# Optimization experiments

Hardware: AMD Instinct MI355X
Metric: run time of the kernel (lower is better)

The kernel has to match this reference:

```python
import jax, jax.numpy as jnp
import numpy as np

B, N, D = 4, 1024, 512      # batch, seq (nodes), input_dim
DK, DV, NH = 512, 512, 8    # dim_k, dim_v, num_heads
EPS = 1e-5


def setup_inputs() -> dict:
    key = jax.random.key(0)
    ks = jax.random.split(key, 9)
    s = 1.0 / np.sqrt(D).astype(np.float32)
    return {
        "user_exo": jax.random.normal(ks[0], (B, N, D), jnp.float32),
        "exo": jax.random.normal(ks[1], (B, N, D), jnp.float32),
        "adj": jax.random.uniform(ks[2], (N, N), jnp.float32),
        "Wq": jax.random.normal(ks[3], (DK, D), jnp.float32) * s,
        "bq": jnp.zeros((DK,), jnp.float32),
        "Wk": jax.random.normal(ks[4], (DK, D), jnp.float32) * s,
        "bk": jnp.zeros((DK,), jnp.float32),
        "Wv": jax.random.normal(ks[5], (DV, D), jnp.float32) * s,
        "bv": jnp.zeros((DV,), jnp.float32),
        "gamma": jnp.ones((D,), jnp.float32),
        "beta": jnp.zeros((D,), jnp.float32),
    }


def reference(user_exo, exo, adj, Wq, bq, Wk, bk, Wv, bv, gamma, beta):
    # LayerNorm over last dim (eps=1e-5, affine)
    mu = jnp.mean(user_exo, axis=-1, keepdims=True)
    var = jnp.mean(jnp.square(user_exo - mu), axis=-1, keepdims=True)
    c = (user_exo - mu) * jax.lax.rsqrt(var + EPS) * gamma + beta

    dk, dv = DK // NH, DV // NH
    # projections -> [B, NH, N, dk/dv]
    q = (jnp.einsum('bnd,kd->bnk', c, Wq) + bq).reshape(B, N, NH, dk).transpose(0, 2, 1, 3)
    k = (jnp.einsum('bnd,kd->bnk', c, Wk) + bk).reshape(B, N, NH, dk).transpose(0, 2, 1, 3)
    v = (jnp.einsum('bnd,kd->bnk', exo, Wv) + bv).reshape(B, N, NH, dv).transpose(0, 2, 1, 3)

    # NOTE: original scales by 1/sqrt(dim_k) (full dim_k, not per-head)
    scale = 1.0 / np.sqrt(DK).astype(np.float32)
    scores = jnp.einsum('bhnd,bhmd->bhnm', q, k) * scale
    dist = jax.nn.softmax(scores, axis=-1)
    # post-softmax multiplicative adjacency mask (mask_local=False path)
    dist = adj * dist  # adj [N,N] broadcasts over [B,NH,N,N]

    att = jnp.einsum('bhnm,bhmd->bhnd', dist, v)
    att = att.transpose(0, 2, 1, 3).reshape(B, N, DV)
    return att, dist
```

## Files before the change

kernel.cpp:

```cpp
#include <hip/hip_runtime.h>
#include <hip/hip_bf16.h>

typedef __hip_bfloat16 bf16;
typedef short v8s __attribute__((ext_vector_type(8)));
typedef float v4f __attribute__((ext_vector_type(4)));

#define BB   4
#define NN   1024
#define DD   512
#define NHH  8
#define DH   64

__device__ __forceinline__ void split2(float v, bf16& hi, bf16& lo) {
    hi = __float2bfloat16(v);
    lo = __float2bfloat16(v - __bfloat162float(hi));
}

__device__ __forceinline__ short f2bf_bits(float f) {
    bf16 h = __float2bfloat16(f);
    short s;
    __builtin_memcpy(&s, &h, 2);
    return s;
}

__global__ __launch_bounds__(256) void ln_split_kernel(
    const float* __restrict__ x, const float* __restrict__ gamma,
    const float* __restrict__ beta,
    bf16* __restrict__ c_hi, bf16* __restrict__ c_lo)
{
    int row = blockIdx.x;
    int t = threadIdx.x;
    const float* xr = x + (size_t)row * DD;
    float v0 = xr[2 * t];
    float v1 = xr[2 * t + 1];
    float s = v0 + v1;
    float sq = v0 * v0 + v1 * v1;
#pragma unroll
    for (int o = 32; o; o >>= 1) {
        s  += __shfl_down(s, o, 64);
        sq += __shfl_down(sq, o, 64);
    }
    __shared__ float red[8];
    __shared__ float mb[2];
    int wave = t >> 6, lane = t & 63;
    if (lane == 0) { red[wave] = s; red[4 + wave] = sq; }
    __syncthreads();
    if (t == 0) {
        float S  = red[0] + red[1] + red[2] + red[3];
        float SQ = red[4] + red[5] + red[6] + red[7];
        float mean = S * (1.0f / DD);
        float var  = SQ * (1.0f / DD) - mean * mean;
        mb[0] = mean;
        mb[1] = rsqrtf(var + 1e-5f);
    }
    __syncthreads();
    float mean = mb[0], rstd = mb[1];
    float y0 = (v0 - mean) * rstd * gamma[2 * t] + beta[2 * t];
    float y1 = (v1 - mean) * rstd * gamma[2 * t + 1] + beta[2 * t + 1];
    bf16 h, l;
    split2(y0, h, l);
    c_hi[(size_t)row * DD + 2 * t]     = h;
    c_lo[(size_t)row * DD + 2 * t]     = l;
    split2(y1, h, l);
    c_hi[(size_t)row * DD + 2 * t + 1] = h;
    c_lo[(size_t)row * DD + 2 * t + 1] = l;
}

__global__ __launch_bounds__(256) void convert_kernel(
    const float* __restrict__ exo, const float* __restrict__ Wq,
    const float* __restrict__ Wk,  const float* __restrict__ Wv,
    bf16* __restrict__ exo_bf,
    bf16* __restrict__ wq_hi, bf16* __restrict__ wq_lo,
    bf16* __restrict__ wk_hi, bf16* __restrict__ wk_lo,
    bf16* __restrict__ wv_bf)
{
    int z = blockIdx.z;
    int n = (z == 0) ? BB * NN * DD : DD * DD;
    int i4 = (blockIdx.x * 256 + threadIdx.x) * 4;
    if (i4 >= n) return;
    const float* src = (z == 0) ? exo : (z == 1) ? Wq : (z == 2) ? Wk : Wv;
    float4 v = *(const float4*)(src + i4);
    float vv[4] = {v.x, v.y, v.z, v.w};
    if (z == 0) {
#pragma unroll
        for (int j = 0; j < 4; ++j) exo_bf[i4 + j] = __float2bfloat16(vv[j]);
        return;
    }
    int col = i4 >> 9;
    int d   = i4 & (DD - 1);
    size_t base = ((size_t)(d >> 5) * DD + col) * 32 + (d & 31);
    if (z == 3) {
#pragma unroll
        for (int j = 0; j < 4; ++j) wv_bf[base + j] = __float2bfloat16(vv[j]);
    } else {
        bf16* dh = (z == 1) ? wq_hi : wk_hi;
        bf16* dl = (z == 1) ? wq_lo : wk_lo;
#pragma unroll
        for (int j = 0; j < 4; ++j) {
            bf16 h, l;
            split2(vv[j], h, l);
            dh[base + j] = h;
            dl[base + j] = l;
        }
    }
}

__global__ __launch_bounds__(256) void proj_kernel(
    const bf16* __restrict__ c_hi, const bf16* __restrict__ c_lo,
    const bf16* __restrict__ exo_bf,
    const bf16* __restrict__ wq_hi, const bf16* __restrict__ wq_lo,
    const bf16* __restrict__ wk_hi, const bf16* __restrict__ wk_lo,
    const bf16* __restrict__ wv_bf,
    const float* __restrict__ bq, const float* __restrict__ bk,
    const float* __restrict__ bv,
    bf16* __restrict__ q_hi, bf16* __restrict__ q_lo,
    bf16* __restrict__ k_hi, bf16* __restrict__ k_lo,
    bf16* __restrict__ vT)
{
    int z = blockIdx.z;
    int lane = threadIdx.x & 63;
    int wave = threadIdx.x >> 6;
    int lr = lane & 15;
    int lq = lane >> 4;
    int row0 = blockIdx.x * 16;
    int colw = wave * 128;

    v4f acc[8] = {};
    if (z < 2) {
        const bf16* Wh = (z == 0) ? wq_hi : wk_hi;
        const bf16* Wl = (z == 0) ? wq_lo : wk_lo;
        const bf16* xh = c_hi + (size_t)(row0 + lr) * DD + lq * 8;
        const bf16* xl = c_lo + (size_t)(row0 + lr) * DD + lq * 8;
        for (int d0 = 0; d0 < DD; d0 += 32) {
            v8s ah = *(const v8s*)(xh + d0);
            v8s al = *(const v8s*)(xl + d0);
            size_t wb = ((size_t)(d0 >> 5) * DD + colw) * 32 + lr * 32 + lq * 8;
#pragma unroll
            for (int t = 0; t < 8; ++t) {
                v8s bh = *(const v8s*)(Wh + wb + (size_t)t * 16 * 32);
                v8s bl = *(const v8s*)(Wl + wb + (size_t)t * 16 * 32);
                acc[t] = __builtin_amdgcn_mfma_f32_16x16x32_bf16(ah, bh, acc[t], 0, 0, 0);
                acc[t] = __builtin_amdgcn_mfma_f32_16x16x32_bf16(al, bh, acc[t], 0, 0, 0);
                acc[t] = __builtin_amdgcn_mfma_f32_16x16x32_bf16(ah, bl, acc[t], 0, 0, 0);
            }
        }
        const float* bias = (z == 0) ? bq : bk;
        bf16* oh = (z == 0) ? q_hi : k_hi;
        bf16* ol = (z == 0) ? q_lo : k_lo;
#pragma unroll
        for (int t = 0; t < 8; ++t) {
            int col = colw + 16 * t + lr;
            float bvv = bias[col];
            int h   = col >> 6;
            int kk2 = (col >> 5) & 1;
            int j   = col & 31;
#pragma unroll
            for (int r = 0; r < 4; ++r) {
                int row = row0 + lq * 4 + r;
                int b_ = row >> 10, n_ = row & (NN - 1);
                size_t idx = ((((size_t)b_ * NHH + h) * 2 + kk2) * NN + n_) * 32 + j;
                float val = acc[t][r] + bvv;
                bf16 hh, ll;
                split2(val, hh, ll);
                oh[idx] = hh;
                ol[idx] = ll;
            }
        }
    } else {
        const bf16* xp = exo_bf + (size_t)(row0 + lr) * DD + lq * 8;
        for (int d0 = 0; d0 < DD; d0 += 32) {
            v8s a = *(const v8s*)(xp + d0);
            size_t wb = ((size_t)(d0 >> 5) * DD + colw) * 32 + lr * 32 + lq * 8;
#pragma unroll
            for (int t = 0; t < 8; ++t) {
                v8s b = *(const v8s*)(wv_bf + wb + (size_t)t * 16 * 32);
                acc[t] = __builtin_amdgcn_mfma_f32_16x16x32_bf16(a, b, acc[t], 0, 0, 0);
            }
        }
#pragma unroll
        for (int t = 0; t < 8; ++t) {
            int col = colw + 16 * t + lr;
            float bvv = bv[col];
#pragma unroll
            for (int r = 0; r < 4; ++r) {
                int row = row0 + lq * 4 + r;
                int b_ = row >> 10, n_ = row & (NN - 1);
                vT[((size_t)b_ * DD + col) * NN + n_] =
                    __float2bfloat16(acc[t][r] + bvv);
            }
        }
    }
}

__global__ __launch_bounds__(256, 4) void attn_fused_kernel(
    const bf16* __restrict__ q_hi, const bf16* __restrict__ q_lo,
    const bf16* __restrict__ k_hi, const bf16* __restrict__ k_lo,
    const float* __restrict__ adj, const bf16* __restrict__ vT,
    float* __restrict__ dist, float* __restrict__ att)
{
    __shared__ __align__(16) short Pb[16][1032];
    __shared__ float redmx[4][16];
    __shared__ float redsm[4][16];

    int i0 = blockIdx.x * 16;
    int h  = blockIdx.y;
    int b  = blockIdx.z;
    int lane = threadIdx.x & 63;
    int wave = threadIdx.x >> 6;
    int lr = lane & 15, lq = lane >> 4;

    const size_t bh2 = (((size_t)b * NHH) + h) * 2;
    const bf16* qhp = q_hi + (bh2 * NN + i0 + lr) * 32 + lq * 8;
    const bf16* qlp = q_lo + (bh2 * NN + i0 + lr) * 32 + lq * 8;
    const bf16* khp = k_hi + bh2 * NN * 32 + lq * 8;
    const bf16* klp = k_lo + bh2 * NN * 32 + lq * 8;

    v4f acc[16] = {};
#pragma unroll
    for (int kk = 0; kk < 2; ++kk) {
        v8s ah = *(const v8s*)(qhp + (size_t)kk * NN * 32);
        v8s al = *(const v8s*)(qlp + (size_t)kk * NN * 32);
#pragma unroll
        for (int t = 0; t < 16; ++t) {
            size_t off = (size_t)(kk * NN + wave * 256 + t * 16 + lr) * 32;
            v8s bh = *(const v8s*)(khp + off);
            v8s bl = *(const v8s*)(klp + off);
            acc[t] = __builtin_amdgcn_mfma_f32_16x16x32_bf16(ah, bh, acc[t], 0, 0, 0);
            acc[t] = __builtin_amdgcn_mfma_f32_16x16x32_bf16(al, bh, acc[t], 0, 0, 0);
            acc[t] = __builtin_amdgcn_mfma_f32_16x16x32_bf16(ah, bl, acc[t], 0, 0, 0);
        }
    }

    float mx[4];
#pragma unroll
    for (int r = 0; r < 4; ++r) {
        float m = acc[0][r];
#pragma unroll
        for (int t = 1; t < 16; ++t) m = fmaxf(m, acc[t][r]);
#pragma unroll
        for (int o = 8; o; o >>= 1) m = fmaxf(m, __shfl_xor(m, o, 64));
        mx[r] = m;
    }
    if (lr == 0) {
#pragma unroll
        for (int r = 0; r < 4; ++r) redmx[wave][lq * 4 + r] = mx[r];
    }
    __syncthreads();
#pragma unroll
    for (int r = 0; r < 4; ++r) {
        float m = fmaxf(fmaxf(redmx[0][lq * 4 + r], redmx[1][lq * 4 + r]),
                        fmaxf(redmx[2][lq * 4 + r], redmx[3][lq * 4 + r]));
        mx[r] = m;
    }

    const float scale = 0.04419417382415922f;
    float sum_[4] = {0.0f, 0.0f, 0.0f, 0.0f};
#pragma unroll
    for (int t = 0; t < 16; ++t) {
#pragma unroll
        for (int r = 0; r < 4; ++r) {
            float e = __expf((acc[t][r] - mx[r]) * scale);
            acc[t][r] = e;
            sum_[r] += e;
        }
    }
#pragma unroll
    for (int r = 0; r < 4; ++r) {
#pragma unroll
        for (int o = 8; o; o >>= 1) sum_[r] += __shfl_xor(sum_[r], o, 64);
    }
    if (lr == 0) {
#pragma unroll
        for (int r = 0; r < 4; ++r) redsm[wave][lq * 4 + r] = sum_[r];
    }
    __syncthreads();
    float inv[4];
#pragma unroll
    for (int r = 0; r < 4; ++r) {
        float s = redsm[0][lq * 4 + r] + redsm[1][lq * 4 + r] +
                  redsm[2][lq * 4 + r] + redsm[3][lq * 4 + r];
        inv[r] = 1.0f / s;
    }

#pragma unroll
    for (int t = 0; t < 16; ++t) {
        int col = wave * 256 + t * 16 + lr;
#pragma unroll
        for (int r = 0; r < 4; ++r) {
            int row = lq * 4 + r;
            int gi = i0 + row;
            float dv = acc[t][r] * inv[r] * adj[(size_t)gi * NN + col];
            __builtin_nontemporal_store(
                dv, dist + ((((size_t)b * NHH + h) * NN) + gi) * NN + col);
            Pb[row][col] = f2bf_bits(dv);
        }
    }
    __syncthreads();

    const bf16* vb = vT + ((size_t)b * DD + h * DH + wave * 16 + lr) * NN + lq * 8;
    v4f acc2 = {};
    for (int m0 = 0; m0 < NN; m0 += 32) {
        v8s a  = *(const v8s*)(&Pb[lr][m0 + lq * 8]);
        v8s bb = *(const v8s*)(vb + m0);
        acc2 = __builtin_amdgcn_mfma_f32_16x16x32_bf16(a, bb, acc2, 0, 0, 0);
    }
#pragma unroll
    for (int r = 0; r < 4; ++r) {
        int row = i0 + lq * 4 + r;
        __builtin_nontemporal_store(
            acc2[r], att + ((size_t)b * NN + row) * DD + h * DH + wave * 16 + lr);
    }
}

extern "C" void kernel_launch(void* const* d_in, const int* in_sizes, int n_in,
                              void* d_out, int out_size, void* d_ws, size_t ws_size,
                              hipStream_t stream)
{
    const float* user_exo = (const float*)d_in[0];
    const float* exo      = (const float*)d_in[1];
    const float* adj      = (const float*)d_in[2];
    const float* Wq       = (const float*)d_in[3];
    const float* bq       = (const float*)d_in[4];
    const float* Wk       = (const float*)d_in[5];
    const float* bk       = (const float*)d_in[6];
    const float* Wv       = (const float*)d_in[7];
    const float* bv       = (const float*)d_in[8];
    const float* gamma    = (const float*)d_in[9];
    const float* beta     = (const float*)d_in[10];

    float* att  = (float*)d_out;
    float* dist = att + (size_t)BB * NN * DD;

    const size_t NE = (size_t)BB * NN * DD;
    const size_t WE = (size_t)DD * DD;
    bf16* p = (bf16*)d_ws;
    bf16* c_hi   = p; p += NE;
    bf16* c_lo   = p; p += NE;
    bf16* exo_bf = p; p += NE;
    bf16* q_hi   = p; p += NE;
    bf16* q_lo   = p; p += NE;
    bf16* k_hi   = p; p += NE;
    bf16* k_lo   = p; p += NE;
    bf16* vT     = p; p += NE;
    bf16* wq_hi  = p; p += WE;
    bf16* wq_lo  = p; p += WE;
    bf16* wk_hi  = p; p += WE;
    bf16* wk_lo  = p; p += WE;
    bf16* wv_bf  = p; p += WE;

    ln_split_kernel<<<BB * NN, 256, 0, stream>>>(user_exo, gamma, beta, c_hi, c_lo);
    convert_kernel<<<dim3((BB * NN * DD / 4 + 255) / 256, 1, 4), 256, 0, stream>>>(
        exo, Wq, Wk, Wv, exo_bf, wq_hi, wq_lo, wk_hi, wk_lo, wv_bf);
    proj_kernel<<<dim3(BB * NN / 16, 1, 3), 256, 0, stream>>>(
        c_hi, c_lo, exo_bf, wq_hi, wq_lo, wk_hi, wk_lo, wv_bf,
        bq, bk, bv, q_hi, q_lo, k_hi, k_lo, vT);
    attn_fused_kernel<<<dim3(NN / 16, NHH, BB), 256, 0, stream>>>(
        q_hi, q_lo, k_hi, k_lo, adj, vT, dist, att);
}
```

Baseline: 294.8 us.

## Stage dist through swizzled LDS for vectorized stores, remap blocks, split projection

The attention kernel now stages the normalized probability tile in a swizzled shared-memory buffer so the large dist output is written with coalesced 16-byte nontemporal stores instead of scattered scalar stores. The att output is staged the same way. The score column mapping is interleaved across waves, and blocks are remapped from a flat 1D grid to group work, probably for cache locality or XCD spreading. The projection kernel's column range is split across two blocks to raise parallelism. In exchange there are extra barriers and LDS traffic, and the LDS buffer shrinks from about 33KB to 32KB.

```diff
diff --git a/kernel.cpp b/kernel.cpp
--- a/kernel.cpp
+++ b/kernel.cpp
@@ -4,24 +4,24 @@
 typedef __hip_bfloat16 bf16;
 typedef short v8s __attribute__((ext_vector_type(8)));
 typedef float v4f __attribute__((ext_vector_type(4)));
+
+__device__ __forceinline__ void split2(float v, bf16& hi, bf16& lo) {
+    hi = __float2bfloat16(v);
+    lo = __float2bfloat16(v - __bfloat162float(hi));
+}
+
+__device__ __forceinline__ short f2bf_bits(float f) {
+    bf16 h = __float2bfloat16(f);
+    short s;
+    __builtin_memcpy(&s, &h, 2);
+    return s;
+}
 
 #define BB   4
 #define NN   1024
 #define DD   512
 #define NHH  8
 #define DH   64
-
-__device__ __forceinline__ void split2(float v, bf16& hi, bf16& lo) {
-    hi = __float2bfloat16(v);
-    lo = __float2bfloat16(v - __bfloat162float(hi));
-}
-
-__device__ __forceinline__ short f2bf_bits(float f) {
-    bf16 h = __float2bfloat16(f);
-    short s;
-    __builtin_memcpy(&s, &h, 2);
-    return s;
-}
 
 __global__ __launch_bounds__(256) void ln_split_kernel(
     const float* __restrict__ x, const float* __restrict__ gamma,
@@ -79,8 +79,8 @@
     int i4 = (blockIdx.x * 256 + threadIdx.x) * 4;
     if (i4 >= n) return;
     const float* src = (z == 0) ? exo : (z == 1) ? Wq : (z == 2) ? Wk : Wv;
-    float4 v = *(const float4*)(src + i4);
-    float vv[4] = {v.x, v.y, v.z, v.w};
+    v4f v = *(const v4f*)(src + i4);
+    float vv[4] = {v[0], v[1], v[2], v[3]};
     if (z == 0) {
 #pragma unroll
         for (int j = 0; j < 4; ++j) exo_bf[i4 + j] = __float2bfloat16(vv[j]);
@@ -123,9 +123,9 @@
     int lr = lane & 15;
     int lq = lane >> 4;
     int row0 = blockIdx.x * 16;
-    int colw = wave * 128;
-
-    v4f acc[8] = {};
+    int colw = blockIdx.y * 256 + wave * 64;
+
+    v4f acc[4] = {};
     if (z < 2) {
         const bf16* Wh = (z == 0) ? wq_hi : wk_hi;
         const bf16* Wl = (z == 0) ? wq_lo : wk_lo;
@@ -136,7 +136,7 @@
             v8s al = *(const v8s*)(xl + d0);
             size_t wb = ((size_t)(d0 >> 5) * DD + colw) * 32 + lr * 32 + lq * 8;
 #pragma unroll
-            for (int t = 0; t < 8; ++t) {
+            for (int t = 0; t < 4; ++t) {
                 v8s bh = *(const v8s*)(Wh + wb + (size_t)t * 16 * 32);
                 v8s bl = *(const v8s*)(Wl + wb + (size_t)t * 16 * 32);
                 acc[t] = __builtin_amdgcn_mfma_f32_16x16x32_bf16(ah, bh, acc[t], 0, 0, 0);
@@ -148,7 +148,7 @@
         bf16* oh = (z == 0) ? q_hi : k_hi;
         bf16* ol = (z == 0) ? q_lo : k_lo;
 #pragma unroll
-        for (int t = 0; t < 8; ++t) {
+        for (int t = 0; t < 4; ++t) {
             int col = colw + 16 * t + lr;
             float bvv = bias[col];
             int h   = col >> 6;
@@ -172,13 +172,13 @@
             v8s a = *(const v8s*)(xp + d0);
             size_t wb = ((size_t)(d0 >> 5) * DD + colw) * 32 + lr * 32 + lq * 8;
 #pragma unroll
-            for (int t = 0; t < 8; ++t) {
+            for (int t = 0; t < 4; ++t) {
                 v8s b = *(const v8s*)(wv_bf + wb + (size_t)t * 16 * 32);
                 acc[t] = __builtin_amdgcn_mfma_f32_16x16x32_bf16(a, b, acc[t], 0, 0, 0);
             }
         }
 #pragma unroll
-        for (int t = 0; t < 8; ++t) {
+        for (int t = 0; t < 4; ++t) {
             int col = colw + 16 * t + lr;
             float bvv = bv[col];
 #pragma unroll
@@ -198,13 +198,14 @@
     const float* __restrict__ adj, const bf16* __restrict__ vT,
     float* __restrict__ dist, float* __restrict__ att)
 {
-    __shared__ __align__(16) short Pb[16][1032];
-    __shared__ float redmx[4][16];
-    __shared__ float redsm[4][16];
-
-    int i0 = blockIdx.x * 16;
-    int h  = blockIdx.y;
-    int b  = blockIdx.z;
+    __shared__ __align__(16) float Sf[16 * 512];
+    short* Pb = (short*)Sf;
+
+    int bid = blockIdx.x;
+    int nid = (bid & 7) * 256 + (bid >> 3);
+    int i0 = (nid & 63) * 16;
+    int h  = (nid >> 6) & 7;
+    int b  = nid >> 9;
     int lane = threadIdx.x & 63;
     int wave = threadIdx.x >> 6;
     int lr = lane & 15, lq = lane >> 4;
@@ -222,7 +223,8 @@
         v8s al = *(const v8s*)(qlp + (size_t)kk * NN * 32);
 #pragma unroll
         for (int t = 0; t < 16; ++t) {
-            size_t off = (size_t)(kk * NN + wave * 256 + t * 16 + lr) * 32;
+            int col = t * 64 + wave * 16 + lr;
+            size_t off = (size_t)(kk * NN + col) * 32;
             v8s bh = *(const v8s*)(khp + off);
             v8s bl = *(const v8s*)(klp + off);
             acc[t] = __builtin_amdgcn_mfma_f32_16x16x32_bf16(ah, bh, acc[t], 0, 0, 0);
@@ -231,6 +233,8 @@
         }
     }
 
+    float* redmx = Sf;
+    float* redsm = Sf + 64;
     float mx[4];
 #pragma unroll
     for (int r = 0; r < 4; ++r) {
@@ -243,14 +247,13 @@
     }
     if (lr == 0) {
 #pragma unroll
-        for (int r = 0; r < 4; ++r) redmx[wave][lq * 4 + r] = mx[r];
+        for (int r = 0; r < 4; ++r) redmx[wave * 16 + lq * 4 + r] = mx[r];
     }
     __syncthreads();
 #pragma unroll
     for (int r = 0; r < 4; ++r) {
-        float m = fmaxf(fmaxf(redmx[0][lq * 4 + r], redmx[1][lq * 4 + r]),
-                        fmaxf(redmx[2][lq * 4 + r], redmx[3][lq * 4 + r]));
-        mx[r] = m;
+        mx[r] = fmaxf(fmaxf(redmx[0 + lq * 4 + r], redmx[16 + lq * 4 + r]),
+                      fmaxf(redmx[32 + lq * 4 + r], redmx[48 + lq * 4 + r]));
     }
 
     const float scale = 0.04419417382415922f;
@@ -271,28 +274,61 @@
     }
     if (lr == 0) {
 #pragma unroll
-        for (int r = 0; r < 4; ++r) redsm[wave][lq * 4 + r] = sum_[r];
+        for (int r = 0; r < 4; ++r) redsm[wave * 16 + lq * 4 + r] = sum_[r];
     }
     __syncthreads();
     float inv[4];
 #pragma unroll
     for (int r = 0; r < 4; ++r) {
-        float s = redsm[0][lq * 4 + r] + redsm[1][lq * 4 + r] +
-                  redsm[2][lq * 4 + r] + redsm[3][lq * 4 + r];
-        inv[r] = 1.0f / s;
+        inv[r] = 1.0f / (redsm[0 + lq * 4 + r] + redsm[16 + lq * 4 + r] +
+                         redsm[32 + lq * 4 + r] + redsm[48 + lq * 4 + r]);
     }
 
 #pragma unroll
     for (int t = 0; t < 16; ++t) {
-        int col = wave * 256 + t * 16 + lr;
+        int col = t * 64 + wave * 16 + lr;
+#pragma unroll
+        for (int r = 0; r < 4; ++r) {
+            int gi = i0 + lq * 4 + r;
+            acc[t][r] = acc[t][r] * inv[r] * adj[(size_t)gi * NN + col];
+        }
+    }
+
+    const size_t drow = ((size_t)(b * NHH + h) * NN + i0) * NN;
+#pragma unroll
+    for (int c = 0; c < 2; ++c) {
+        __syncthreads();
+#pragma unroll
+        for (int tt = 0; tt < 8; ++tt) {
+            int t = 8 * c + tt;
+            int lcol = tt * 64 + wave * 16 + lr;
+#pragma unroll
+            for (int r = 0; r < 4; ++r) {
+                int row = lq * 4 + r;
+                Sf[row * 512 + (lcol ^ ((row & 7) << 2))] = acc[t][r];
+            }
+        }
+        __syncthreads();
+#pragma unroll
+        for (int j = 0; j < 8; ++j) {
+            int f = j * 256 + threadIdx.x;
+            int row = f >> 7;
+            int col4 = f & 127;
+            v4f val = *(const v4f*)(Sf + row * 512 +
+                                    ((col4 * 4) ^ ((row & 7) << 2)));
+            __builtin_nontemporal_store(
+                val, (v4f*)(dist + drow + (size_t)row * NN + c * 512 + col4 * 4));
+        }
+    }
+    __syncthreads();
+
+#pragma unroll
+    for (int t = 0; t < 16; ++t) {
+        int col = t * 64 + wave * 16 + lr;
 #pragma unroll
         for (int r = 0; r < 4; ++r) {
             int row = lq * 4 + r;
-            int gi = i0 + row;
-            float dv = acc[t][r] * inv[r] * adj[(size_t)gi * NN + col];
-            __builtin_nontemporal_store(
-                dv, dist + ((((size_t)b * NHH + h) * NN) + gi) * NN + col);
-            Pb[row][col] = f2bf_bits(dv);
+            Pb[row * 1024 + (col ^ ((row & 7) << 3))] = f2bf_bits(acc[t][r]);
         }
     }
     __syncthreads();
@@ -300,15 +336,23 @@
     const bf16* vb = vT + ((size_t)b * DD + h * DH + wave * 16 + lr) * NN + lq * 8;
     v4f acc2 = {};
     for (int m0 = 0; m0 < NN; m0 += 32) {
-        v8s a  = *(const v8s*)(&Pb[lr][m0 + lq * 8]);
+        int e = (m0 + lq * 8) ^ ((lr & 7) << 3);
+        v8s a  = *(const v8s*)(Pb + lr * 1024 + e);
         v8s bb = *(const v8s*)(vb + m0);
         acc2 = __builtin_amdgcn_mfma_f32_16x16x32_bf16(a, bb, acc2, 0, 0, 0);
     }
-#pragma unroll
-    for (int r = 0; r < 4; ++r) {
-        int row = i0 + lq * 4 + r;
+
+    __syncthreads();
+#pragma unroll
+    for (int r = 0; r < 4; ++r)
+        Sf[(lq * 4 + r) * 64 + wave * 16 + lr] = acc2[r];
+    __syncthreads();
+    {
+        int row = threadIdx.x >> 4;
+        int col4 = threadIdx.x & 15;
+        v4f val = *(const v4f*)(Sf + row * 64 + col4 * 4);
         __builtin_nontemporal_store(
-            acc2[r], att + ((size_t)b * NN + row) * DD + h * DH + wave * 16 + lr);
+            val, (v4f*)(att + ((size_t)b * NN + i0 + row) * DD + h * DH + col4 * 4));
     }
 }
 
@@ -351,9 +395,9 @@
     ln_split_kernel<<<BB * NN, 256, 0, stream>>>(user_exo, gamma, beta, c_hi, c_lo);
     convert_kernel<<<dim3((BB * NN * DD / 4 + 255) / 256, 1, 4), 256, 0, stream>>>(
         exo, Wq, Wk, Wv, exo_bf, wq_hi, wq_lo, wk_hi, wk_lo, wv_bf);
-    proj_kernel<<<dim3(BB * NN / 16, 1, 3), 256, 0, stream>>>(
+    proj_kernel<<<dim3(BB * NN / 16, 2, 3), 256, 0, stream>>>(
         c_hi, c_lo, exo_bf, wq_hi, wq_lo, wk_hi, wk_lo, wv_bf,
         bq, bk, bv, q_hi, q_lo, k_hi, k_lo, vT);
-    attn_fused_kernel<<<dim3(NN / 16, NHH, BB), 256, 0, stream>>>(
+    attn_fused_kernel<<<dim3(BB * NHH * (NN / 16)), 256, 0, stream>>>(
         q_hi, q_lo, k_hi, k_lo, adj, vT, dist, att);
 }
```

Result: slower. 350.9 us (+19.1%).

## Transpose softmax probabilities through LDS for vectorized adj loads and dist stores

Applied to the files above, without the earlier changes.

The dist/adj epilogue used to do scalar per-element global loads and nontemporal stores with lane-strided columns. It now stages each wave's normalized softmax tile in XOR-swizzled shared memory, reads it back row-contiguous, and multiplies by adj using float4 loads and float4 nontemporal stores. The bf16 P matrix for the PV MFMA is packed as 4-element stores into a swizzled per-wave layout, and the PV loop is unrolled. The cost is extra LDS traffic and register pressure from holding 16 v4f values, which may hurt occupancy.

```diff
diff --git a/kernel.cpp b/kernel.cpp
--- a/kernel.cpp
+++ b/kernel.cpp
@@ -4,24 +4,25 @@
 typedef __hip_bfloat16 bf16;
 typedef short v8s __attribute__((ext_vector_type(8)));
 typedef float v4f __attribute__((ext_vector_type(4)));
+typedef unsigned int v2u __attribute__((ext_vector_type(2)));
+
+__device__ __forceinline__ void split2(float v, bf16& hi, bf16& lo) {
+    hi = __float2bfloat16(v);
+    lo = __float2bfloat16(v - __bfloat162float(hi));
+}
+
+__device__ __forceinline__ unsigned short f2bf_bits(float f) {
+    bf16 h = __float2bfloat16(f);
+    unsigned short s;
+    __builtin_memcpy(&s, &h, 2);
+    return s;
+}
 
 #define BB   4
 #define NN   1024
 #define DD   512
 #define NHH  8
 #define DH   64
-
-__device__ __forceinline__ void split2(float v, bf16& hi, bf16& lo) {
-    hi = __float2bfloat16(v);
-    lo = __float2bfloat16(v - __bfloat162float(hi));
-}
-
-__device__ __forceinline__ short f2bf_bits(float f) {
-    bf16 h = __float2bfloat16(f);
-    short s;
-    __builtin_memcpy(&s, &h, 2);
-    return s;
-}
 
 __global__ __launch_bounds__(256) void ln_split_kernel(
     const float* __restrict__ x, const float* __restrict__ gamma,
@@ -79,8 +80,8 @@
     int i4 = (blockIdx.x * 256 + threadIdx.x) * 4;
     if (i4 >= n) return;
     const float* src = (z == 0) ? exo : (z == 1) ? Wq : (z == 2) ? Wk : Wv;
-    float4 v = *(const float4*)(src + i4);
-    float vv[4] = {v.x, v.y, v.z, v.w};
+    v4f v = *(const v4f*)(src + i4);
+    float vv[4] = {v[0], v[1], v[2], v[3]};
     if (z == 0) {
 #pragma unroll
         for (int j = 0; j < 4; ++j) exo_bf[i4 + j] = __float2bfloat16(vv[j]);
@@ -198,9 +199,10 @@
     const float* __restrict__ adj, const bf16* __restrict__ vT,
     float* __restrict__ dist, float* __restrict__ att)
 {
-    __shared__ __align__(16) short Pb[16][1032];
-    __shared__ float redmx[4][16];
-    __shared__ float redsm[4][16];
+    __shared__ __align__(16) float Sf[4 * 2048];
+    __shared__ float redmx[64];
+    __shared__ float redsm[64];
+    short* PbS = (short*)Sf;
 
     int i0 = blockIdx.x * 16;
     int h  = blockIdx.y;
@@ -243,14 +245,13 @@
     }
     if (lr == 0) {
 #pragma unroll
-        for (int r = 0; r < 4; ++r) redmx[wave][lq * 4 + r] = mx[r];
-    }
-    __syncthreads();
-#pragma unroll
-    for (int r = 0; r < 4; ++r) {
-        float m = fmaxf(fmaxf(redmx[0][lq * 4 + r], redmx[1][lq * 4 + r]),
-                        fmaxf(redmx[2][lq * 4 + r], redmx[3][lq * 4 + r]));
-        mx[r] = m;
+        for (int r = 0; r < 4; ++r) redmx[wave * 16 + lq * 4 + r] = mx[r];
+    }
+    __syncthreads();
+#pragma unroll
+    for (int r = 0; r < 4; ++r) {
+        mx[r] = fmaxf(fmaxf(redmx[0 + lq * 4 + r], redmx[16 + lq * 4 + r]),
+                      fmaxf(redmx[32 + lq * 4 + r], redmx[48 + lq * 4 + r]));
     }
 
     const float scale = 0.04419417382415922f;
@@ -271,36 +272,69 @@
     }
     if (lr == 0) {
 #pragma unroll
-        for (int r = 0; r < 4; ++r) redsm[wave][lq * 4 + r] = sum_[r];
+        for (int r = 0; r < 4; ++r) redsm[wave * 16 + lq * 4 + r] = sum_[r];
     }
     __syncthreads();
     float inv[4];
 #pragma unroll
     for (int r = 0; r < 4; ++r) {
-        float s = redsm[0][lq * 4 + r] + redsm[1][lq * 4 + r] +
-                  redsm[2][lq * 4 + r] + redsm[3][lq * 4 + r];
-        inv[r] = 1.0f / s;
-    }
-
+        inv[r] = 1.0f / (redsm[0 + lq * 4 + r] + redsm[16 + lq * 4 + r] +
+                         redsm[32 + lq * 4 + r] + redsm[48 + lq * 4 + r]);
+    }
 #pragma unroll
     for (int t = 0; t < 16; ++t) {
-        int col = wave * 256 + t * 16 + lr;
-#pragma unroll
-        for (int r = 0; r < 4; ++r) {
-            int row = lq * 4 + r;
+#pragma unroll
+        for (int r = 0; r < 4; ++r) acc[t][r] *= inv[r];
+    }
+
+    float* Sw = Sf + wave * 2048;
+    const size_t drow = ((size_t)(b * NHH + h) * NN + i0) * NN;
+    v4f rv[16];
+#pragma unroll
+    for (int P = 0; P < 2; ++P) {
+#pragma unroll
+        for (int rrr = 0; rrr < 2; ++rrr) {
+            int slot = rrr * 4 + lq;
+#pragma unroll
+            for (int t = 0; t < 16; ++t) {
+                Sw[slot * 256 + ((t * 16 + lr) ^ (slot << 3))] = acc[t][2 * P + rrr];
+            }
+        }
+        asm volatile("s_waitcnt lgkmcnt(0)" ::: "memory");
+#pragma unroll
+        for (int j = 0; j < 8; ++j) {
+            int row = (j & 3) * 4 + 2 * P + (j >> 2);
             int gi = i0 + row;
-            float dv = acc[t][r] * inv[r] * adj[(size_t)gi * NN + col];
+            v4f sv = *(const v4f*)(Sw + j * 256 + ((lane * 4) ^ (j << 3)));
+            v4f av = *(const v4f*)(adj + (size_t)gi * NN + wave * 256 + lane * 4);
+            v4f dv = sv * av;
             __builtin_nontemporal_store(
-                dv, dist + ((((size_t)b * NHH + h) * NN) + gi) * NN + col);
-            Pb[row][col] = f2bf_bits(dv);
-        }
+                dv, (v4f*)(dist + drow + (size_t)row * NN + wave * 256 + lane * 4));
+            rv[P * 8 + j] = dv;
+        }
+        asm volatile("" ::: "memory");
+    }
+
+#pragma unroll
+    for (int k16 = 0; k16 < 16; ++k16) {
+        int j = k16 & 7;
+        int row = (j & 3) * 4 + 2 * (k16 >> 3) + (j >> 2);
+        v4f dv = rv[k16];
+        unsigned int lo = (unsigned int)f2bf_bits(dv[0]) |
+                          ((unsigned int)f2bf_bits(dv[1]) << 16);
+        unsigned int hi = (unsigned int)f2bf_bits(dv[2]) |
+                          ((unsigned int)f2bf_bits(dv[3]) << 16);
+        v2u pk = {lo, hi};
+        *(v2u*)(PbS + wave * 4096 + row * 256 + ((lane * 4) ^ ((row & 7) << 3))) = pk;
     }
     __syncthreads();
 
     const bf16* vb = vT + ((size_t)b * DD + h * DH + wave * 16 + lr) * NN + lq * 8;
     v4f acc2 = {};
+#pragma unroll
     for (int m0 = 0; m0 < NN; m0 += 32) {
-        v8s a  = *(const v8s*)(&Pb[lr][m0 + lq * 8]);
+        v8s a = *(const v8s*)(PbS + (m0 >> 8) * 4096 + lr * 256 +
+                              (((m0 & 255) + lq * 8) ^ ((lr & 7) << 3)));
         v8s bb = *(const v8s*)(vb + m0);
         acc2 = __builtin_amdgcn_mfma_f32_16x16x32_bf16(a, bb, acc2, 0, 0, 0);
     }
```

Measured after the change: 298.8 us. Within noise of the previous version (+1.4%).
